# Performance work log

Hardware: AMD Instinct MI355X
Metric: run time of the kernel (lower is better)

Reference implementation:

```python
import jax, jax.numpy as jnp
import numpy as np

B, S, D, H = 2, 2048, 1024, 16
DH = D // H  # per-head attention dim


def setup_inputs() -> dict:
    key = jax.random.key(0)
    ks = jax.random.split(key, 11)
    scale = 0.02
    return {
        "query": jax.random.normal(ks[0], (B, S, D), jnp.float32),
        "key": jax.random.normal(ks[1], (B, S, D), jnp.float32),
        "value": jax.random.normal(ks[2], (B, S, D), jnp.float32),
        # per-head QKV projection weights, stacked over heads: [H, D, DH]
        "Wq": jax.random.normal(ks[3], (H, D, DH), jnp.float32) * scale,
        "bq": jnp.zeros((H, DH), jnp.float32),
        "Wk": jax.random.normal(ks[4], (H, D, DH), jnp.float32) * scale,
        "bk": jnp.zeros((H, DH), jnp.float32),
        "Wv": jax.random.normal(ks[5], (H, D, DH), jnp.float32) * scale,
        "bv": jnp.zeros((H, DH), jnp.float32),
        # output linear: [D, D]
        "Wo": jax.random.normal(ks[6], (D, D), jnp.float32) * scale,
        "bo": jnp.zeros((D,), jnp.float32),
        "look_ahead_mask": 1,
    }


def reference(query, key, value, Wq, bq, Wk, bk, Wv, bv, Wo, bo, look_ahead_mask):
    # batched per-head projections: [B,S,D] x [H,D,E] -> [B,H,S,E]
    q = jnp.einsum("bsd,hde->bhse", query, Wq) + bq[None, :, None, :]
    k = jnp.einsum("bsd,hde->bhse", key, Wk) + bk[None, :, None, :]
    v = jnp.einsum("bsd,hde->bhse", value, Wv) + bv[None, :, None, :]
    scores = jnp.einsum("bhqe,bhke->bhqk", q, k) / jnp.sqrt(jnp.float32(DH))
    if look_ahead_mask:
        causal = jnp.tril(jnp.ones((S, S), bool))
        scores = jnp.where(causal[None, None], scores, jnp.float32(-1e9))
    probs = jax.nn.softmax(scores, axis=-1)
    ctx = jnp.einsum("bhqk,bhke->bhqe", probs, v)  # [B,H,S,DH]
    # concat heads along last dim (head order matches ModuleList order)
    concat = ctx.transpose(0, 2, 1, 3).reshape(B, S, D)
    return concat @ Wo + bo
```

## Files before the change

kernel.cpp:

```cpp
#include <hip/hip_runtime.h>


typedef short bf16x8 __attribute__((ext_vector_type(8)));
typedef float f32x4 __attribute__((ext_vector_type(4)));

__device__ __forceinline__ unsigned short f2bf(float f){
  unsigned int u = __builtin_bit_cast(unsigned int, f);
  u = (u + 0x7fffu + ((u >> 16) & 1u)) >> 16;
  return (unsigned short)u;
}

__device__ __forceinline__ void gld_lds16(const void* src, void* dst){
  __builtin_amdgcn_global_load_lds((const __attribute__((address_space(1))) unsigned int*)src,
                                   (__attribute__((address_space(3))) unsigned int*)dst,
                                   16, 0, 0);
}

__device__ __forceinline__ void stage_lds(const char* gtile, size_t growb, char* lds,
                                          int tid, int rowb_lg2, int swz, int tilebytes){
  int w = tid >> 6;
  for (int c = 0; c < tilebytes; c += 4096){
    int o = c + tid*16;
    int row = o >> rowb_lg2;
    int colb = o & ((1 << rowb_lg2) - 1);
    if (swz) colb ^= ((row & 7) << 4);
    gld_lds16(gtile + (size_t)row*growb + colb, lds + c + w*1024);
  }
}

__global__ __launch_bounds__(256) void convertx(const float* __restrict__ in,
                                                unsigned short* __restrict__ out, int n8){
  int i = blockIdx.x*blockDim.x + threadIdx.x;
  if (i >= n8) return;
  const float4* p = (const float4*)in;
  float4 a = p[2*i], b = p[2*i+1];
  uint4 o;
  o.x = (unsigned int)f2bf(a.x) | ((unsigned int)f2bf(a.y) << 16);
  o.y = (unsigned int)f2bf(a.z) | ((unsigned int)f2bf(a.w) << 16);
  o.z = (unsigned int)f2bf(b.x) | ((unsigned int)f2bf(b.y) << 16);
  o.w = (unsigned int)f2bf(b.z) | ((unsigned int)f2bf(b.w) << 16);
  ((uint4*)out)[i] = o;
}

__global__ __launch_bounds__(256) void transpose_bf16(const float* __restrict__ in,
                                                      unsigned short* __restrict__ out,
                                                      int R, int C,
                                                      size_t in_mstride, size_t out_mstride){
  __shared__ unsigned short tile[64][66];
  int t = threadIdx.x;
  int r0 = blockIdx.x*64, c0 = blockIdx.y*64;
  const float* inm = in + (size_t)blockIdx.z*in_mstride;
  unsigned short* outm = out + (size_t)blockIdx.z*out_mstride;
  int j = t & 63, i0 = (t >> 6)*16;
  #pragma unroll
  for (int ii = 0; ii < 16; ii++){
    int i = i0 + ii;
    tile[i][j] = f2bf(inm[(size_t)(r0+i)*C + c0 + j]);
  }
  __syncthreads();
  #pragma unroll
  for (int ii = 0; ii < 16; ii++){
    int i = i0 + ii;
    outm[(size_t)(c0+i)*R + r0 + j] = tile[j][i];
  }
}

template<int EPI>
__global__ __launch_bounds__(256) void gemm_bt(const unsigned short* __restrict__ A,
                                               const unsigned short* __restrict__ BT,
                                               const float* __restrict__ bias,
                                               void* __restrict__ outp,
                                               int M, int N, int K, float scale){
  __shared__ __align__(16) unsigned short lA[2][128*32];
  __shared__ __align__(16) unsigned short lB[2][128*32];
  int tid = threadIdx.x, lane = tid & 63, w = tid >> 6;
  int bn = blockIdx.x*128, bm = blockIdx.y*128;
  int wm = (w >> 1)*64, wn = (w & 1)*64;
  int lr = lane & 15;
  int lkb = (lane >> 4)*16;
  const char* Ab = (const char*)(A + (size_t)bm*K);
  const char* Bb = (const char*)(BT + (size_t)bn*K);
  size_t grow = (size_t)K*2;
  int nk = K >> 5;

  f32x4 zf = {0.f,0.f,0.f,0.f};
  f32x4 acc[4][4];
  #pragma unroll
  for (int mi = 0; mi < 4; mi++)
    #pragma unroll
    for (int ni = 0; ni < 4; ni++) acc[mi][ni] = zf;

  stage_lds(Ab, grow, (char*)lA[0], tid, 6, 0, 8192);
  stage_lds(Bb, grow, (char*)lB[0], tid, 6, 0, 8192);
  __syncthreads();
  int cur = 0;
  for (int kt = 0; kt < nk; kt++){
    if (kt + 1 < nk){
      stage_lds(Ab + (size_t)(kt+1)*64, grow, (char*)lA[cur^1], tid, 6, 0, 8192);
      stage_lds(Bb + (size_t)(kt+1)*64, grow, (char*)lB[cur^1], tid, 6, 0, 8192);
    }
    const char* pa = (const char*)lA[cur];
    const char* pb = (const char*)lB[cur];
    bf16x8 af[4], bfr[4];
    #pragma unroll
    for (int mi = 0; mi < 4; mi++)
      af[mi] = *(const bf16x8*)(pa + (wm + mi*16 + lr)*64 + lkb);
    #pragma unroll
    for (int ni = 0; ni < 4; ni++)
      bfr[ni] = *(const bf16x8*)(pb + (wn + ni*16 + lr)*64 + lkb);
    #pragma unroll
    for (int mi = 0; mi < 4; mi++)
      #pragma unroll
      for (int ni = 0; ni < 4; ni++)
        acc[mi][ni] = __builtin_amdgcn_mfma_f32_16x16x32_bf16(af[mi], bfr[ni], acc[mi][ni], 0, 0, 0);
    __syncthreads();
    cur ^= 1;
  }

  #pragma unroll
  for (int mi = 0; mi < 4; mi++)
    #pragma unroll
    for (int ni = 0; ni < 4; ni++)
      #pragma unroll
      for (int r = 0; r < 4; r++){
        int row = bm + wm + mi*16 + (lane >> 4)*4 + r;
        int col = bn + wn + ni*16 + (lane & 15);
        float v = acc[mi][ni][r] + bias[col];
        if (EPI == 0){
          v *= scale;
          unsigned short* o = (unsigned short*)outp;
          o[(size_t)((row >> 11)*16 + (col >> 6))*131072 + (size_t)(row & 2047)*64 + (col & 63)] = f2bf(v);
        } else {
          float* o = (float*)outp;
          o[(size_t)row*N + col] = v;
        }
      }
}

__global__ __launch_bounds__(256) void attn_fwd(const unsigned short* __restrict__ qh,
                                                const unsigned short* __restrict__ kh,
                                                const unsigned short* __restrict__ vh,
                                                unsigned short* __restrict__ cc,
                                                const int* __restrict__ maskp){
  __shared__ __align__(16) unsigned short Qs[128*64];
  __shared__ __align__(16) unsigned short Ks[64*64];
  __shared__ __align__(16) unsigned short VTs[64*64];
  __shared__ __align__(16) unsigned short Ps[4][32*64];
  int tid = threadIdx.x, lane = tid & 63, w = tid >> 6;
  int lg = lane >> 4, lr = lane & 15;
  int qt = blockIdx.x, bh = blockIdx.y;
  size_t base = (size_t)bh * (2048*64);
  const unsigned short* Q = qh + base;
  const unsigned short* K = kh + base;
  const unsigned short* V = vh + base;
  int q0 = qt*128;
  int causal = *maskp;

  stage_lds((const char*)(Q + (size_t)q0*64), 128, (char*)Qs, tid, 7, 1, 16384);
  __syncthreads();

  bf16x8 qf[2][2];
  #pragma unroll
  for (int mi = 0; mi < 2; mi++)
    #pragma unroll
    for (int kk = 0; kk < 2; kk++){
      int row = w*32 + mi*16 + lr;
      qf[mi][kk] = *(const bf16x8*)((const char*)Qs + row*128 + ((kk*64 + lg*16) ^ ((row & 7) << 4)));
    }

  f32x4 zf = {0.f,0.f,0.f,0.f};
  f32x4 oa[2][4];
  float mr[2][4], lsm[2][4];
  #pragma unroll
  for (int mi = 0; mi < 2; mi++){
    #pragma unroll
    for (int ei = 0; ei < 4; ei++) oa[mi][ei] = zf;
    #pragma unroll
    for (int r = 0; r < 4; r++){ mr[mi][r] = -1e30f; lsm[mi][r] = 0.f; }
  }

  int nt = causal ? (q0/64 + 2) : 32;
  int wq0 = q0 + w*32;

  for (int t = 0; t < nt; t++){
    __syncthreads();
    stage_lds((const char*)(K + (size_t)t*4096), 128, (char*)Ks, tid, 7, 1, 8192);
    #pragma unroll
    for (int c = 0; c < 2; c++){
      int o = c*4096 + tid*16;
      uint4 vvv = *(const uint4*)((const char*)V + (size_t)t*8192 + o);
      int kv = o >> 7;
      int e0 = (o & 127) >> 1;
      unsigned int uu[4] = {vvv.x, vvv.y, vvv.z, vvv.w};
      #pragma unroll
      for (int j = 0; j < 4; j++){
        int e1 = e0 + 2*j, e2 = e1 + 1;
        *(unsigned short*)((char*)VTs + e1*128 + ((kv*2) ^ ((e1 & 7) << 4))) = (unsigned short)(uu[j] & 0xffffu);
        *(unsigned short*)((char*)VTs + e2*128 + ((kv*2) ^ ((e2 & 7) << 4))) = (unsigned short)(uu[j] >> 16);
      }
    }
    __syncthreads();

    if (causal && (t*64 > wq0 + 31)) continue;

    f32x4 sc[2][4];
    #pragma unroll
    for (int mi = 0; mi < 2; mi++)
      #pragma unroll
      for (int ni = 0; ni < 4; ni++) sc[mi][ni] = zf;
    #pragma unroll
    for (int kk = 0; kk < 2; kk++)
      #pragma unroll
      for (int ni = 0; ni < 4; ni++){
        int krow = ni*16 + lr;
        bf16x8 kf = *(const bf16x8*)((const char*)Ks + krow*128 + ((kk*64 + lg*16) ^ ((krow & 7) << 4)));
        #pragma unroll
        for (int mi = 0; mi < 2; mi++)
          sc[mi][ni] = __builtin_amdgcn_mfma_f32_16x16x32_bf16(qf[mi][kk], kf, sc[mi][ni], 0, 0, 0);
      }

    if (causal && (t*64 + 63 > wq0)){
      #pragma unroll
      for (int mi = 0; mi < 2; mi++)
        #pragma unroll
        for (int ni = 0; ni < 4; ni++)
          #pragma unroll
          for (int r = 0; r < 4; r++){
            int qrow = wq0 + mi*16 + lg*4 + r;
            int kvc  = t*64 + ni*16 + lr;
            if (kvc > qrow) sc[mi][ni][r] = -1e9f;
          }
    }

    #pragma unroll
    for (int mi = 0; mi < 2; mi++)
      #pragma unroll
      for (int r = 0; r < 4; r++){
        float mx = fmaxf(fmaxf(sc[mi][0][r], sc[mi][1][r]), fmaxf(sc[mi][2][r], sc[mi][3][r]));
        #pragma unroll
        for (int off = 1; off < 16; off <<= 1)
          mx = fmaxf(mx, __shfl_xor(mx, off, 64));
        float mo = mr[mi][r];
        float mn = fmaxf(mo, mx);
        mr[mi][r] = mn;
        float alpha = __expf(mo - mn);
        float psum = 0.f;
        #pragma unroll
        for (int ni = 0; ni < 4; ni++){
          float p = __expf(sc[mi][ni][r] - mn);
          sc[mi][ni][r] = p;
          psum += p;
        }
        #pragma unroll
        for (int off = 1; off < 16; off <<= 1)
          psum += __shfl_xor(psum, off, 64);
        lsm[mi][r] = lsm[mi][r]*alpha + psum;
        #pragma unroll
        for (int ei = 0; ei < 4; ei++) oa[mi][ei][r] *= alpha;
      }

    #pragma unroll
    for (int mi = 0; mi < 2; mi++)
      #pragma unroll
      for (int ni = 0; ni < 4; ni++)
        #pragma unroll
        for (int r = 0; r < 4; r++){
          int prow = mi*16 + lg*4 + r;
          int pcb = (ni*16 + lr)*2;
          *(unsigned short*)((char*)Ps[w] + prow*128 + (pcb ^ ((prow & 7) << 4))) = f2bf(sc[mi][ni][r]);
        }

    #pragma unroll
    for (int kk = 0; kk < 2; kk++){
      bf16x8 pf[2];
      #pragma unroll
      for (int mi = 0; mi < 2; mi++){
        int prow = mi*16 + lr;
        pf[mi] = *(const bf16x8*)((const char*)Ps[w] + prow*128 + ((kk*64 + lg*16) ^ ((prow & 7) << 4)));
      }
      #pragma unroll
      for (int ei = 0; ei < 4; ei++){
        int vrow = ei*16 + lr;
        bf16x8 vf = *(const bf16x8*)((const char*)VTs + vrow*128 + ((kk*64 + lg*16) ^ ((vrow & 7) << 4)));
        #pragma unroll
        for (int mi = 0; mi < 2; mi++)
          oa[mi][ei] = __builtin_amdgcn_mfma_f32_16x16x32_bf16(pf[mi], vf, oa[mi][ei], 0, 0, 0);
      }
    }
  }

  int b = bh >> 4, h = bh & 15;
  #pragma unroll
  for (int mi = 0; mi < 2; mi++)
    #pragma unroll
    for (int r = 0; r < 4; r++){
      float inv = 1.f / lsm[mi][r];
      int q = q0 + w*32 + mi*16 + lg*4 + r;
      size_t rowbase = (size_t)(b*2048 + q)*1024 + h*64;
      #pragma unroll
      for (int ei = 0; ei < 4; ei++){
        int e = ei*16 + lr;
        cc[rowbase + e] = f2bf(oa[mi][ei][r] * inv);
      }
    }
}

extern "C" void kernel_launch(void* const* d_in, const int* in_sizes, int n_in,
                              void* d_out, int out_size, void* d_ws, size_t ws_size,
                              hipStream_t stream){
  const float* query = (const float*)d_in[0];
  const float* key_i = (const float*)d_in[1];
  const float* value = (const float*)d_in[2];
  const float* Wq = (const float*)d_in[3];
  const float* bq = (const float*)d_in[4];
  const float* Wk = (const float*)d_in[5];
  const float* bk = (const float*)d_in[6];
  const float* Wv = (const float*)d_in[7];
  const float* bv = (const float*)d_in[8];
  const float* Wo = (const float*)d_in[9];
  const float* bo = (const float*)d_in[10];
  const int* mask = (const int*)d_in[11];

  char* ws = (char*)d_ws;
  const size_t ACT = 8388608;
  unsigned short* Xq  = (unsigned short*)(ws + 0*ACT);
  unsigned short* Xk  = (unsigned short*)(ws + 1*ACT);
  unsigned short* Xv  = (unsigned short*)(ws + 2*ACT);
  unsigned short* qh  = (unsigned short*)(ws + 3*ACT);
  unsigned short* kh  = (unsigned short*)(ws + 4*ACT);
  unsigned short* vh  = (unsigned short*)(ws + 5*ACT);
  unsigned short* cc  = (unsigned short*)(ws + 6*ACT);
  unsigned short* WqT = (unsigned short*)(ws + 7*ACT);
  unsigned short* WkT = (unsigned short*)(ws + 7*ACT + 2097152);
  unsigned short* WvT = (unsigned short*)(ws + 7*ACT + 4194304);
  unsigned short* WoT = (unsigned short*)(ws + 7*ACT + 6291456);

  convertx<<<2048, 256, 0, stream>>>(query, Xq, 524288);
  convertx<<<2048, 256, 0, stream>>>(key_i, Xk, 524288);
  convertx<<<2048, 256, 0, stream>>>(value, Xv, 524288);

  transpose_bf16<<<dim3(16,1,16), 256, 0, stream>>>(Wq, WqT, 1024, 64, 65536, 65536);
  transpose_bf16<<<dim3(16,1,16), 256, 0, stream>>>(Wk, WkT, 1024, 64, 65536, 65536);
  transpose_bf16<<<dim3(16,1,16), 256, 0, stream>>>(Wv, WvT, 1024, 64, 65536, 65536);
  transpose_bf16<<<dim3(16,16,1), 256, 0, stream>>>(Wo, WoT, 1024, 1024, 0, 0);

  gemm_bt<0><<<dim3(8,32), 256, 0, stream>>>(Xq, WqT, bq, qh, 4096, 1024, 1024, 0.125f);
  gemm_bt<0><<<dim3(8,32), 256, 0, stream>>>(Xk, WkT, bk, kh, 4096, 1024, 1024, 1.0f);
  gemm_bt<0><<<dim3(8,32), 256, 0, stream>>>(Xv, WvT, bv, vh, 4096, 1024, 1024, 1.0f);

  attn_fwd<<<dim3(16,32), 256, 0, stream>>>(qh, kh, vh, cc, mask);

  gemm_bt<1><<<dim3(8,32), 256, 0, stream>>>(cc, WoT, bo, d_out, 4096, 1024, 1024, 1.0f);
}
```

Baseline: 364.3 us.

## Batch QKV GEMMs and conversions into single launches; halve attention query tile

Merges the three input conversion kernels into one launch and the three QKV projection GEMMs into one grid with a z dimension of 3. The attention kernel now processes 64 query rows per block instead of 128, giving each wave 16 rows and doubling the grid to 1024 blocks. This raises parallelism and helps balance the causal workload across blocks. The trade-off is that each K/V tile is loaded and V transposed twice as many times per head, and each wave does less MFMA work per staging barrier.

Measured after the change: 359.3 us. About the same (-1.4%).

```diff
diff --git a/kernel.cpp b/kernel.cpp
--- a/kernel.cpp
+++ b/kernel.cpp
@@ -28,18 +28,24 @@
   }
 }
 
-__global__ __launch_bounds__(256) void convertx(const float* __restrict__ in,
-                                                unsigned short* __restrict__ out, int n8){
+__global__ __launch_bounds__(256) void convert3(const float* __restrict__ a,
+                                                const float* __restrict__ b,
+                                                const float* __restrict__ c,
+                                                unsigned short* __restrict__ outa,
+                                                unsigned short* __restrict__ outb,
+                                                unsigned short* __restrict__ outc){
   int i = blockIdx.x*blockDim.x + threadIdx.x;
-  if (i >= n8) return;
+  int seg = i >> 19, il = i & 524287;
+  const float* in = seg==0 ? a : (seg==1 ? b : c);
+  unsigned short* out = seg==0 ? outa : (seg==1 ? outb : outc);
   const float4* p = (const float4*)in;
-  float4 a = p[2*i], b = p[2*i+1];
+  float4 x = p[2*il], y = p[2*il+1];
   uint4 o;
-  o.x = (unsigned int)f2bf(a.x) | ((unsigned int)f2bf(a.y) << 16);
-  o.y = (unsigned int)f2bf(a.z) | ((unsigned int)f2bf(a.w) << 16);
-  o.z = (unsigned int)f2bf(b.x) | ((unsigned int)f2bf(b.y) << 16);
-  o.w = (unsigned int)f2bf(b.z) | ((unsigned int)f2bf(b.w) << 16);
-  ((uint4*)out)[i] = o;
+  o.x = (unsigned int)f2bf(x.x) | ((unsigned int)f2bf(x.y) << 16);
+  o.y = (unsigned int)f2bf(x.z) | ((unsigned int)f2bf(x.w) << 16);
+  o.z = (unsigned int)f2bf(y.x) | ((unsigned int)f2bf(y.y) << 16);
+  o.w = (unsigned int)f2bf(y.z) | ((unsigned int)f2bf(y.w) << 16);
+  ((uint4*)out)[il] = o;
 }
 
 __global__ __launch_bounds__(256) void transpose_bf16(const float* __restrict__ in,
@@ -66,13 +72,10 @@
 }
 
 template<int EPI>
-__global__ __launch_bounds__(256) void gemm_bt(const unsigned short* __restrict__ A,
-                                               const unsigned short* __restrict__ BT,
-                                               const float* __restrict__ bias,
-                                               void* __restrict__ outp,
-                                               int M, int N, int K, float scale){
-  __shared__ __align__(16) unsigned short lA[2][128*32];
-  __shared__ __align__(16) unsigned short lB[2][128*32];
+__device__ __forceinline__ void gemm_body(const unsigned short* A, const unsigned short* BT,
+                                          const float* bias, void* outp, float scale,
+                                          unsigned short (*lA)[128*32], unsigned short (*lB)[128*32]){
+  const int K = 1024, N = 1024;
   int tid = threadIdx.x, lane = tid & 63, w = tid >> 6;
   int bn = blockIdx.x*128, bm = blockIdx.y*128;
   int wm = (w >> 1)*64, wn = (w & 1)*64;
@@ -137,15 +140,47 @@
       }
 }
 
+__global__ __launch_bounds__(256) void gemm_qkv(const unsigned short* __restrict__ Xq,
+                                                const unsigned short* __restrict__ Xk,
+                                                const unsigned short* __restrict__ Xv,
+                                                const unsigned short* __restrict__ WqT,
+                                                const unsigned short* __restrict__ WkT,
+                                                const unsigned short* __restrict__ WvT,
+                                                const float* __restrict__ bq,
+                                                const float* __restrict__ bk,
+                                                const float* __restrict__ bv,
+                                                unsigned short* __restrict__ oq,
+                                                unsigned short* __restrict__ ok,
+                                                unsigned short* __restrict__ ov){
+  __shared__ __align__(16) unsigned short lA[2][128*32];
+  __shared__ __align__(16) unsigned short lB[2][128*32];
+  int z = blockIdx.z;
+  const unsigned short* A  = z==0 ? Xq  : (z==1 ? Xk  : Xv);
+  const unsigned short* BT = z==0 ? WqT : (z==1 ? WkT : WvT);
+  const float* bias        = z==0 ? bq  : (z==1 ? bk  : bv);
+  unsigned short* out      = z==0 ? oq  : (z==1 ? ok  : ov);
+  float scale = z==0 ? 0.125f : 1.0f;
+  gemm_body<0>(A, BT, bias, out, scale, lA, lB);
+}
+
+__global__ __launch_bounds__(256) void gemm_out(const unsigned short* __restrict__ A,
+                                                const unsigned short* __restrict__ BT,
+                                                const float* __restrict__ bias,
+                                                float* __restrict__ outp){
+  __shared__ __align__(16) unsigned short lA[2][128*32];
+  __shared__ __align__(16) unsigned short lB[2][128*32];
+  gemm_body<1>(A, BT, bias, outp, 1.0f, lA, lB);
+}
+
 __global__ __launch_bounds__(256) void attn_fwd(const unsigned short* __restrict__ qh,
                                                 const unsigned short* __restrict__ kh,
                                                 const unsigned short* __restrict__ vh,
                                                 unsigned short* __restrict__ cc,
                                                 const int* __restrict__ maskp){
-  __shared__ __align__(16) unsigned short Qs[128*64];
+  __shared__ __align__(16) unsigned short Qs[64*64];
   __shared__ __align__(16) unsigned short Ks[64*64];
   __shared__ __align__(16) unsigned short VTs[64*64];
-  __shared__ __align__(16) unsigned short Ps[4][32*64];
+  __shared__ __align__(16) unsigned short Ps[4][16*64];
   int tid = threadIdx.x, lane = tid & 63, w = tid >> 6;
   int lg = lane >> 4, lr = lane & 15;
   int qt = blockIdx.x, bh = blockIdx.y;
@@ -153,34 +188,29 @@
   const unsigned short* Q = qh + base;
   const unsigned short* K = kh + base;
   const unsigned short* V = vh + base;
-  int q0 = qt*128;
+  int q0 = qt*64;
   int causal = *maskp;
 
-  stage_lds((const char*)(Q + (size_t)q0*64), 128, (char*)Qs, tid, 7, 1, 16384);
+  stage_lds((const char*)(Q + (size_t)q0*64), 128, (char*)Qs, tid, 7, 1, 8192);
   __syncthreads();
 
-  bf16x8 qf[2][2];
-  #pragma unroll
-  for (int mi = 0; mi < 2; mi++)
-    #pragma unroll
-    for (int kk = 0; kk < 2; kk++){
-      int row = w*32 + mi*16 + lr;
-      qf[mi][kk] = *(const bf16x8*)((const char*)Qs + row*128 + ((kk*64 + lg*16) ^ ((row & 7) << 4)));
-    }
+  bf16x8 qf[2];
+  #pragma unroll
+  for (int kk = 0; kk < 2; kk++){
+    int row = w*16 + lr;
+    qf[kk] = *(const bf16x8*)((const char*)Qs + row*128 + ((kk*64 + lg*16) ^ ((row & 7) << 4)));
+  }
 
   f32x4 zf = {0.f,0.f,0.f,0.f};
-  f32x4 oa[2][4];
-  float mr[2][4], lsm[2][4];
-  #pragma unroll
-  for (int mi = 0; mi < 2; mi++){
-    #pragma unroll
-    for (int ei = 0; ei < 4; ei++) oa[mi][ei] = zf;
-    #pragma unroll
-    for (int r = 0; r < 4; r++){ mr[mi][r] = -1e30f; lsm[mi][r] = 0.f; }
-  }
-
-  int nt = causal ? (q0/64 + 2) : 32;
-  int wq0 = q0 + w*32;
+  f32x4 oa[4];
+  float mr[4], lsm[4];
+  #pragma unroll
+  for (int ei = 0; ei < 4; ei++) oa[ei] = zf;
+  #pragma unroll
+  for (int r = 0; r < 4; r++){ mr[r] = -1e30f; lsm[r] = 0.f; }
+
+  int nt = causal ? (qt + 1) : 32;
+  int wq0 = q0 + w*16;
 
   for (int t = 0; t < nt; t++){
     __syncthreads();
@@ -201,108 +231,89 @@
     }
     __syncthreads();
 
-    if (causal && (t*64 > wq0 + 31)) continue;
-
-    f32x4 sc[2][4];
-    #pragma unroll
-    for (int mi = 0; mi < 2; mi++)
-      #pragma unroll
-      for (int ni = 0; ni < 4; ni++) sc[mi][ni] = zf;
+    if (causal && (t*64 > wq0 + 15)) continue;
+
+    f32x4 sc[4];
+    #pragma unroll
+    for (int ni = 0; ni < 4; ni++) sc[ni] = zf;
     #pragma unroll
     for (int kk = 0; kk < 2; kk++)
       #pragma unroll
       for (int ni = 0; ni < 4; ni++){
         int krow = ni*16 + lr;
         bf16x8 kf = *(const bf16x8*)((const char*)Ks + krow*128 + ((kk*64 + lg*16) ^ ((krow & 7) << 4)));
-        #pragma unroll
-        for (int mi = 0; mi < 2; mi++)
-          sc[mi][ni] = __builtin_amdgcn_mfma_f32_16x16x32_bf16(qf[mi][kk], kf, sc[mi][ni], 0, 0, 0);
+        sc[ni] = __builtin_amdgcn_mfma_f32_16x16x32_bf16(qf[kk], kf, sc[ni], 0, 0, 0);
       }
 
     if (causal && (t*64 + 63 > wq0)){
-      #pragma unroll
-      for (int mi = 0; mi < 2; mi++)
-        #pragma unroll
-        for (int ni = 0; ni < 4; ni++)
-          #pragma unroll
-          for (int r = 0; r < 4; r++){
-            int qrow = wq0 + mi*16 + lg*4 + r;
-            int kvc  = t*64 + ni*16 + lr;
-            if (kvc > qrow) sc[mi][ni][r] = -1e9f;
-          }
-    }
-
-    #pragma unroll
-    for (int mi = 0; mi < 2; mi++)
-      #pragma unroll
-      for (int r = 0; r < 4; r++){
-        float mx = fmaxf(fmaxf(sc[mi][0][r], sc[mi][1][r]), fmaxf(sc[mi][2][r], sc[mi][3][r]));
-        #pragma unroll
-        for (int off = 1; off < 16; off <<= 1)
-          mx = fmaxf(mx, __shfl_xor(mx, off, 64));
-        float mo = mr[mi][r];
-        float mn = fmaxf(mo, mx);
-        mr[mi][r] = mn;
-        float alpha = __expf(mo - mn);
-        float psum = 0.f;
-        #pragma unroll
-        for (int ni = 0; ni < 4; ni++){
-          float p = __expf(sc[mi][ni][r] - mn);
-          sc[mi][ni][r] = p;
-          psum += p;
-        }
-        #pragma unroll
-        for (int off = 1; off < 16; off <<= 1)
-          psum += __shfl_xor(psum, off, 64);
-        lsm[mi][r] = lsm[mi][r]*alpha + psum;
-        #pragma unroll
-        for (int ei = 0; ei < 4; ei++) oa[mi][ei][r] *= alpha;
-      }
-
-    #pragma unroll
-    for (int mi = 0; mi < 2; mi++)
       #pragma unroll
       for (int ni = 0; ni < 4; ni++)
         #pragma unroll
         for (int r = 0; r < 4; r++){
-          int prow = mi*16 + lg*4 + r;
-          int pcb = (ni*16 + lr)*2;
-          *(unsigned short*)((char*)Ps[w] + prow*128 + (pcb ^ ((prow & 7) << 4))) = f2bf(sc[mi][ni][r]);
+          int qrow = wq0 + lg*4 + r;
+          int kvc  = t*64 + ni*16 + lr;
+          if (kvc > qrow) sc[ni][r] = -1e9f;
         }
+    }
+
+    #pragma unroll
+    for (int r = 0; r < 4; r++){
+      float mx = fmaxf(fmaxf(sc[0][r], sc[1][r]), fmaxf(sc[2][r], sc[3][r]));
+      #pragma unroll
+      for (int off = 1; off < 16; off <<= 1)
+        mx = fmaxf(mx, __shfl_xor(mx, off, 64));
+      float mo = mr[r];
+      float mn = fmaxf(mo, mx);
+      mr[r] = mn;
+      float alpha = __expf(mo - mn);
+      float psum = 0.f;
+      #pragma unroll
+      for (int ni = 0; ni < 4; ni++){
+        float p = __expf(sc[ni][r] - mn);
+        sc[ni][r] = p;
+        psum += p;
+      }
+      #pragma unroll
+      for (int off = 1; off < 16; off <<= 1)
+        psum += __shfl_xor(psum, off, 64);
+      lsm[r] = lsm[r]*alpha + psum;
+      #pragma unroll
+      for (int ei = 0; ei < 4; ei++) oa[ei][r] *= alpha;
+    }
+
+    #pragma unroll
+    for (int ni = 0; ni < 4; ni++)
+      #pragma unroll
+      for (int r = 0; r < 4; r++){
+        int prow = lg*4 + r;
+        int pcb = (ni*16 + lr)*2;
+        *(unsigned short*)((char*)Ps[w] + prow*128 + (pcb ^ ((prow & 7) << 4))) = f2bf(sc[ni][r]);
+      }
 
     #pragma unroll
     for (int kk = 0; kk < 2; kk++){
-      bf16x8 pf[2];
-      #pragma unroll
-      for (int mi = 0; mi < 2; mi++){
-        int prow = mi*16 + lr;
-        pf[mi] = *(const bf16x8*)((const char*)Ps[w] + prow*128 + ((kk*64 + lg*16) ^ ((prow & 7) << 4)));
-      }
+      bf16x8 pf = *(const bf16x8*)((const char*)Ps[w] + lr*128 + ((kk*64 + lg*16) ^ ((lr & 7) << 4)));
       #pragma unroll
       for (int ei = 0; ei < 4; ei++){
         int vrow = ei*16 + lr;
         bf16x8 vf = *(const bf16x8*)((const char*)VTs + vrow*128 + ((kk*64 + lg*16) ^ ((vrow & 7) << 4)));
-        #pragma unroll
-        for (int mi = 0; mi < 2; mi++)
-          oa[mi][ei] = __builtin_amdgcn_mfma_f32_16x16x32_bf16(pf[mi], vf, oa[mi][ei], 0, 0, 0);
+        oa[ei] = __builtin_amdgcn_mfma_f32_16x16x32_bf16(pf, vf, oa[ei], 0, 0, 0);
       }
     }
   }
 
   int b = bh >> 4, h = bh & 15;
   #pragma unroll
-  for (int mi = 0; mi < 2; mi++)
-    #pragma unroll
-    for (int r = 0; r < 4; r++){
-      float inv = 1.f / lsm[mi][r];
-      int q = q0 + w*32 + mi*16 + lg*4 + r;
-      size_t rowbase = (size_t)(b*2048 + q)*1024 + h*64;
-      #pragma unroll
-      for (int ei = 0; ei < 4; ei++){
-        int e = ei*16 + lr;
-        cc[rowbase + e] = f2bf(oa[mi][ei][r] * inv);
-      }
-    }
+  for (int r = 0; r < 4; r++){
+    float inv = 1.f / lsm[r];
+    int q = q0 + w*16 + lg*4 + r;
+    size_t rowbase = (size_t)(b*2048 + q)*1024 + h*64;
+    #pragma unroll
+    for (int ei = 0; ei < 4; ei++){
+      int e = ei*16 + lr;
+      cc[rowbase + e] = f2bf(oa[ei][r] * inv);
+    }
+  }
 }
 
 extern "C" void kernel_launch(void* const* d_in, const int* in_sizes, int n_in,
@@ -335,20 +346,16 @@
   unsigned short* WvT = (unsigned short*)(ws + 7*ACT + 4194304);
   unsigned short* WoT = (unsigned short*)(ws + 7*ACT + 6291456);
 
-  convertx<<<2048, 256, 0, stream>>>(query, Xq, 524288);
-  convertx<<<2048, 256, 0, stream>>>(key_i, Xk, 524288);
-  convertx<<<2048, 256, 0, stream>>>(value, Xv, 524288);
+  convert3<<<6144, 256, 0, stream>>>(query, key_i, value, Xq, Xk, Xv);
 
   transpose_bf16<<<dim3(16,1,16), 256, 0, stream>>>(Wq, WqT, 1024, 64, 65536, 65536);
   transpose_bf16<<<dim3(16,1,16), 256, 0, stream>>>(Wk, WkT, 1024, 64, 65536, 65536);
   transpose_bf16<<<dim3(16,1,16), 256, 0, stream>>>(Wv, WvT, 1024, 64, 65536, 65536);
   transpose_bf16<<<dim3(16,16,1), 256, 0, stream>>>(Wo, WoT, 1024, 1024, 0, 0);
 
-  gemm_bt<0><<<dim3(8,32), 256, 0, stream>>>(Xq, WqT, bq, qh, 4096, 1024, 1024, 0.125f);
-  gemm_bt<0><<<dim3(8,32), 256, 0, stream>>>(Xk, WkT, bk, kh, 4096, 1024, 1024, 1.0f);
-  gemm_bt<0><<<dim3(8,32), 256, 0, stream>>>(Xv, WvT, bv, vh, 4096, 1024, 1024, 1.0f);
-
-  attn_fwd<<<dim3(16,32), 256, 0, stream>>>(qh, kh, vh, cc, mask);
-
-  gemm_bt<1><<<dim3(8,32), 256, 0, stream>>>(cc, WoT, bo, d_out, 4096, 1024, 1024, 1.0f);
-}
+  gemm_qkv<<<dim3(8,32,3), 256, 0, stream>>>(Xq, Xk, Xv, WqT, WkT, WvT, bq, bk, bv, qh, kh, vh);
+
+  attn_fwd<<<dim3(32,32), 256, 0, stream>>>(qh, kh, vh, cc, mask);
+
+  gemm_out<<<dim3(8,32), 256, 0, stream>>>(cc, WoT, bo, (float*)d_out);
+}
```
